# Optimization experiments

Hardware: AMD Instinct MI355X
Metric: run time of the kernel (lower is better)

Reference implementation:

```python
import jax, jax.numpy as jnp
import numpy as np

# ---- static config (must match init_kwargs) ----
DIM = 256
DIM_K = 16
N = 32          # window size: hh = ww = N
HEADS = 8
DIM_OUT = 256
DIM_U = 1
DIM_V = DIM_OUT // HEADS  # 32
EPS = 1e-5
N2 = N * N


def _calc_rel_pos(n):
    # pos: (n*n, 2) of (i, j) coords, rel: (n*n, n*n, 2) shifted by n-1
    pos = np.stack(np.meshgrid(np.arange(n), np.arange(n), indexing='ij'), axis=-1).reshape(-1, 2)
    rel = pos[None, :, :] - pos[:, None, :] + (n - 1)
    return rel.astype(np.int32)

_REL = _calc_rel_pos(N)  # (N2, N2, 2)


def _cplx(re, im):
    return jax.lax.complex(re, im)


def _complex_bn(x, scale, shift):
    # x: (b, c, m) complex. Complex batchnorm: var = E[x^2] - E[x]^2 (complex square).
    mean = x.mean(axis=(0, 2))                       # (c,)
    var = (x ** 2).mean(axis=(0, 2)) - mean ** 2     # (c,) complex
    xn = (x - mean[None, :, None]) / jnp.sqrt(var + EPS)[None, :, None]
    return scale[None, :, None] * xn + shift[None, :, None]


def setup_inputs() -> dict:
    key = jax.random.key(0)
    ks = jax.random.split(key, 18)
    f = jnp.float32
    b = 16
    mk = lambda k, shape, s=1.0: (jax.random.normal(k, shape, dtype=f) * s)
    inp = {
        'x_re': mk(ks[0], (b, DIM, N, N)),
        'x_im': mk(ks[1], (b, DIM, N, N)),
        # 1x1 conv weights, stored as (out_ch, in_ch)
        'wq_re': mk(ks[2], (DIM_K * HEADS, DIM), DIM ** -0.5),
        'wq_im': mk(ks[3], (DIM_K * HEADS, DIM), DIM ** -0.5),
        'wk_re': mk(ks[4], (DIM_K * DIM_U, DIM), DIM ** -0.5),
        'wk_im': mk(ks[5], (DIM_K * DIM_U, DIM), DIM ** -0.5),
        'wv_re': mk(ks[6], (DIM_V * DIM_U, DIM), DIM ** -0.5),
        'wv_im': mk(ks[7], (DIM_V * DIM_U, DIM), DIM ** -0.5),
        # complex BN affine params (init: scale=1+0j, shift=0)
        'qs_re': jnp.ones((DIM_K * HEADS,), f),
        'qs_im': jnp.zeros((DIM_K * HEADS,), f),
        'qb_re': jnp.zeros((DIM_K * HEADS,), f),
        'qb_im': jnp.zeros((DIM_K * HEADS,), f),
        'vs_re': jnp.ones((DIM_V * DIM_U,), f),
        'vs_im': jnp.zeros((DIM_V * DIM_U,), f),
        'vb_re': jnp.zeros((DIM_V * DIM_U,), f),
        'vb_im': jnp.zeros((DIM_V * DIM_U,), f),
        # rel-pos embedding table (2n-1, 2n-1, k, u)
        'emb_re': mk(ks[8], (2 * N - 1, 2 * N - 1, DIM_K, DIM_U)),
        'emb_im': mk(ks[9], (2 * N - 1, 2 * N - 1, DIM_K, DIM_U)),
    }
    return inp


def reference(x_re, x_im, wq_re, wq_im, wk_re, wk_im, wv_re, wv_im,
              qs_re, qs_im, qb_re, qb_im, vs_re, vs_im, vb_re, vb_im,
              emb_re, emb_im):
    x = _cplx(x_re, x_im)                       # (b, c, N, N)
    b = x.shape[0]
    xf = x.reshape(b, DIM, N2)                  # (b, c, m)

    wq = _cplx(wq_re, wq_im)
    wk = _cplx(wk_re, wk_im)
    wv = _cplx(wv_re, wv_im)

    q = jnp.einsum('oc,bcm->bom', wq, xf)       # (b, k*h, m)
    k = jnp.einsum('oc,bcm->bom', wk, xf)       # (b, k*u, m)
    v = jnp.einsum('oc,bcm->bom', wv, xf)       # (b, v*u, m)

    q = _complex_bn(q, _cplx(qs_re, qs_im), _cplx(qb_re, qb_im))
    v = _complex_bn(v, _cplx(vs_re, vs_im), _cplx(vb_re, vb_im))

    q = q.reshape(b, HEADS, DIM_K, N2)          # b h k n
    k = k.reshape(b, DIM_U, DIM_K, N2)          # b u k m
    v = v.reshape(b, DIM_U, DIM_V, N2)          # b u v m

    k = jax.nn.softmax(jnp.abs(k), axis=-1).astype(jnp.complex64)

    lam_c = jnp.einsum('bukm,buvm->bkv', k, v)          # content lambda
    Yc = jnp.einsum('bhkn,bkv->bhvn', q, lam_c)

    emb = _cplx(emb_re, emb_im)
    remb = emb[_REL[..., 0], _REL[..., 1]]              # (n, m, k, u) gathered
    lam_p = jnp.einsum('nmku,buvm->bnkv', remb, v)      # positional lambdas
    Yp = jnp.einsum('bhkn,bnkv->bhvn', q, lam_p)

    Y = Yc + Yp                                          # (b, h, v, n)
    out = Y.reshape(b, HEADS * DIM_V, N, N)             # b (h v) hh ww
    return out
```

## Files before the change

kernel.cpp:

```cpp
#include <hip/hip_runtime.h>
#include <math.h>

#define DIMC 256
#define NCH  176
#define MM   1024
#define BB   16
#define KD   16
#define HH   8
#define VD   32
#define EPSV 1e-5
#define OPAD 192

typedef short short8 __attribute__((ext_vector_type(8)));
typedef float f32x4  __attribute__((ext_vector_type(4)));
typedef unsigned u32x4v __attribute__((ext_vector_type(4)));

union frag8 { unsigned u[4]; short8 s; u32x4v v; };

__device__ __forceinline__ unsigned bf16rne(float f) {
    unsigned u = __float_as_uint(f);
    unsigned r = u + 0x7FFFu + ((u >> 16) & 1u);
    return r >> 16;
}
__device__ __forceinline__ float bf16tof(unsigned h) {
    return __uint_as_float(h << 16);
}

#define GL2LDS16(g, l) __builtin_amdgcn_global_load_lds( \
    (const __attribute__((address_space(1))) unsigned*)(g), \
    (__attribute__((address_space(3))) unsigned*)(l), 16, 0, 0)

__global__ __launch_bounds__(256) void k_wprep(
    const float* __restrict__ wq_re, const float* __restrict__ wq_im,
    const float* __restrict__ wk_re, const float* __restrict__ wk_im,
    const float* __restrict__ wv_re, const float* __restrict__ wv_im,
    unsigned* __restrict__ Wpk)
{
    int idx = blockIdx.x * 256 + threadIdx.x;
    if (idx >= OPAD * 128) return;
    int o = idx >> 7, j = idx & 127;
    int c0 = 2 * j;
    float r0 = 0.f, r1 = 0.f, i0 = 0.f, i1 = 0.f;
    if (o < 128) {
        r0 = wq_re[o * DIMC + c0]; r1 = wq_re[o * DIMC + c0 + 1];
        i0 = wq_im[o * DIMC + c0]; i1 = wq_im[o * DIMC + c0 + 1];
    } else if (o < 144) {
        int oo = o - 128;
        r0 = wk_re[oo * DIMC + c0]; r1 = wk_re[oo * DIMC + c0 + 1];
        i0 = wk_im[oo * DIMC + c0]; i1 = wk_im[oo * DIMC + c0 + 1];
    } else if (o < 176) {
        int oo = o - 144;
        r0 = wv_re[oo * DIMC + c0]; r1 = wv_re[oo * DIMC + c0 + 1];
        i0 = wv_im[oo * DIMC + c0]; i1 = wv_im[oo * DIMC + c0 + 1];
    }
    unsigned rh0 = bf16rne(r0), rh1 = bf16rne(r1);
    unsigned ih0 = bf16rne(i0), ih1 = bf16rne(i1);
    float rl0 = r0 - bf16tof(rh0), rl1 = r1 - bf16tof(rh1);
    float il0 = i0 - bf16tof(ih0), il1 = i1 - bf16tof(ih1);
    Wpk[0 * OPAD * 128 + idx] = rh0 | (rh1 << 16);
    Wpk[1 * OPAD * 128 + idx] = ih0 | (ih1 << 16);
    Wpk[2 * OPAD * 128 + idx] = bf16rne(rl0) | (bf16rne(rl1) << 16);
    Wpk[3 * OPAD * 128 + idx] = bf16rne(il0) | (bf16rne(il1) << 16);
}

__global__ __launch_bounds__(256, 2) void k_proj(
    const float* __restrict__ x_re, const float* __restrict__ x_im,
    const unsigned* __restrict__ Wpk,
    float2* __restrict__ O)
{
    const int m0  = blockIdx.x * 32;
    const int b   = blockIdx.y;
    const int tid = threadIdx.x;
    const int w    = tid >> 6;
    const int lane = tid & 63;
    const int quad = lane >> 4;
    const int col  = lane & 15;
    const int mt = w & 1, og = w >> 1;

    __shared__ __align__(16) unsigned Wsh[4 * OPAD * 16];
    __shared__ __align__(16) unsigned Xsh[4 * 32 * 20];

    f32x4 accR[6], accI[6];
#pragma unroll
    for (int t = 0; t < 6; ++t) {
        accR[t] = (f32x4){0.f, 0.f, 0.f, 0.f};
        accI[t] = (f32x4){0.f, 0.f, 0.f, 0.f};
    }

    const int cl = tid >> 3;
    const int m4 = (tid & 7) * 4;
    const int cp = cl >> 1, half = cl & 1;

#pragma unroll 1
    for (int kk = 0; kk < 8; ++kk) {
#pragma unroll
        for (int p = 0; p < 12; ++p) {
            int idx = p * 256 + tid;
            int plane = idx / 768;
            int rem = idx - plane * 768;
            int row = rem >> 2, seg = rem & 3;
            u32x4v d = *(const u32x4v*)&Wpk[(size_t)plane * (OPAD * 128) + row * 128 + kk * 16 + seg * 4];
            *(u32x4v*)&Wsh[(plane * OPAD + row) * 16 + seg * 4] = d;
        }
        {
            size_t base = ((size_t)(b * DIMC + kk * 32 + cl)) * MM + m0 + m4;
            float4 xr = *(const float4*)&x_re[base];
            float4 xi = *(const float4*)&x_im[base];
            unsigned short* xs = (unsigned short*)Xsh;
            const float* xrf = (const float*)&xr;
            const float* xif = (const float*)&xi;
#pragma unroll
            for (int j = 0; j < 4; ++j) {
                float r = xrf[j], iv = xif[j];
                unsigned rh = bf16rne(r), ih = bf16rne(iv);
                float rl = r - bf16tof(rh), il = iv - bf16tof(ih);
                int m = m4 + j;
                xs[(0 * 640 + m * 20 + cp) * 2 + half] = (unsigned short)rh;
                xs[(1 * 640 + m * 20 + cp) * 2 + half] = (unsigned short)ih;
                xs[(2 * 640 + m * 20 + cp) * 2 + half] = (unsigned short)bf16rne(rl);
                xs[(3 * 640 + m * 20 + cp) * 2 + half] = (unsigned short)bf16rne(il);
            }
        }
        __syncthreads();

        int mrow = mt * 16 + col;
        short8 Xrh = *(const short8*)&Xsh[0 * 640 + mrow * 20 + quad * 4];
        short8 Xih = *(const short8*)&Xsh[1 * 640 + mrow * 20 + quad * 4];
        short8 Xrl = *(const short8*)&Xsh[2 * 640 + mrow * 20 + quad * 4];
        short8 Xil = *(const short8*)&Xsh[3 * 640 + mrow * 20 + quad * 4];

#pragma unroll
        for (int ot = 0; ot < 6; ++ot) {
            int orow = (og * 6 + ot) * 16 + col;
            frag8 Arh, Aih, Arl, Ail, Anh, Anl;
            Arh.s = *(const short8*)&Wsh[(0 * OPAD + orow) * 16 + quad * 4];
            Aih.s = *(const short8*)&Wsh[(1 * OPAD + orow) * 16 + quad * 4];
            Arl.s = *(const short8*)&Wsh[(2 * OPAD + orow) * 16 + quad * 4];
            Ail.s = *(const short8*)&Wsh[(3 * OPAD + orow) * 16 + quad * 4];
#pragma unroll
            for (int i = 0; i < 4; ++i) {
                Anh.u[i] = Aih.u[i] ^ 0x80008000u;
                Anl.u[i] = Ail.u[i] ^ 0x80008000u;
            }
            accR[ot] = __builtin_amdgcn_mfma_f32_16x16x32_bf16(Arh.s, Xrh, accR[ot], 0, 0, 0);
            accR[ot] = __builtin_amdgcn_mfma_f32_16x16x32_bf16(Anh.s, Xih, accR[ot], 0, 0, 0);
            accR[ot] = __builtin_amdgcn_mfma_f32_16x16x32_bf16(Arh.s, Xrl, accR[ot], 0, 0, 0);
            accR[ot] = __builtin_amdgcn_mfma_f32_16x16x32_bf16(Anh.s, Xil, accR[ot], 0, 0, 0);
            accR[ot] = __builtin_amdgcn_mfma_f32_16x16x32_bf16(Arl.s, Xrh, accR[ot], 0, 0, 0);
            accR[ot] = __builtin_amdgcn_mfma_f32_16x16x32_bf16(Anl.s, Xih, accR[ot], 0, 0, 0);
            accI[ot] = __builtin_amdgcn_mfma_f32_16x16x32_bf16(Arh.s, Xih, accI[ot], 0, 0, 0);
            accI[ot] = __builtin_amdgcn_mfma_f32_16x16x32_bf16(Aih.s, Xrh, accI[ot], 0, 0, 0);
            accI[ot] = __builtin_amdgcn_mfma_f32_16x16x32_bf16(Arh.s, Xil, accI[ot], 0, 0, 0);
            accI[ot] = __builtin_amdgcn_mfma_f32_16x16x32_bf16(Aih.s, Xrl, accI[ot], 0, 0, 0);
            accI[ot] = __builtin_amdgcn_mfma_f32_16x16x32_bf16(Arl.s, Xih, accI[ot], 0, 0, 0);
            accI[ot] = __builtin_amdgcn_mfma_f32_16x16x32_bf16(Ail.s, Xrh, accI[ot], 0, 0, 0);
        }
        __syncthreads();
    }

#pragma unroll
    for (int ot = 0; ot < 6; ++ot) {
        int gto = og * 6 + ot;
        if (gto >= 11) continue;
#pragma unroll
        for (int r = 0; r < 4; ++r) {
            int o = gto * 16 + quad * 4 + r;
            O[((size_t)(b * NCH + o)) * MM + m0 + mt * 16 + col] =
                make_float2(accR[ot][r], accI[ot][r]);
        }
    }
}

__global__ __launch_bounds__(256) void k_bnstats(
    const float2* __restrict__ O,
    const float* __restrict__ qs_re, const float* __restrict__ qs_im,
    const float* __restrict__ qb_re, const float* __restrict__ qb_im,
    const float* __restrict__ vs_re, const float* __restrict__ vs_im,
    const float* __restrict__ vb_re, const float* __restrict__ vb_im,
    float4* __restrict__ stats)
{
    const int ch  = blockIdx.x;
    const int o   = (ch < 128) ? ch : (144 + ch - 128);
    const int tid = threadIdx.x;

    double sr = 0, si = 0, sq = 0, sri = 0;
    for (int idx = tid; idx < BB * MM; idx += 256) {
        int b = idx >> 10, m = idx & 1023;
        float2 val = O[((size_t)(b * NCH + o)) * MM + m];
        double r = val.x, ii = val.y;
        sr += r; si += ii; sq += r * r - ii * ii; sri += r * ii;
    }
    __shared__ double red[4][256];
    red[0][tid] = sr; red[1][tid] = si; red[2][tid] = sq; red[3][tid] = sri;
    __syncthreads();
    for (int s = 128; s > 0; s >>= 1) {
        if (tid < s) {
            red[0][tid] += red[0][tid + s]; red[1][tid] += red[1][tid + s];
            red[2][tid] += red[2][tid + s]; red[3][tid] += red[3][tid + s];
        }
        __syncthreads();
    }
    if (tid == 0) {
        const double inv = 1.0 / (double)(BB * MM);
        double mr = red[0][0] * inv, mi = red[1][0] * inv;
        double vr = red[2][0] * inv - (mr * mr - mi * mi) + EPSV;
        double vi = 2.0 * (red[3][0] * inv - mr * mi);
        double rad = sqrt(vr * vr + vi * vi);
        double wr  = sqrt(fmax(0.5 * (rad + vr), 0.0));
        double wi  = sqrt(fmax(0.5 * (rad - vr), 0.0));
        if (vi < 0) wi = -wi;
        double den = wr * wr + wi * wi;
        double ivr = wr / den, ivi = -wi / den;
        double scr, sci, shr, shi;
        if (ch < 128) { scr = qs_re[ch]; sci = qs_im[ch]; shr = qb_re[ch]; shi = qb_im[ch]; }
        else { int i2 = ch - 128; scr = vs_re[i2]; sci = vs_im[i2]; shr = vb_re[i2]; shi = vb_im[i2]; }
        double Ar = scr * ivr - sci * ivi;
        double Ai = scr * ivi + sci * ivr;
        double Br = shr - (Ar * mr - Ai * mi);
        double Bi = shi - (Ar * mi + Ai * mr);
        stats[ch] = make_float4((float)Ar, (float)Ai, (float)Br, (float)Bi);
    }
}

__global__ __launch_bounds__(256) void k_bnapply(
    const float4* __restrict__ stats, float2* __restrict__ O,
    unsigned* __restrict__ VR, unsigned* __restrict__ VI)
{
    int ch = blockIdx.x, b = blockIdx.y;
    int o  = (ch < 128) ? ch : (144 + ch - 128);
    float4 s = stats[ch];
    float2* row = O + ((size_t)(b * NCH + o)) * MM;
    int tid = threadIdx.x;
    for (int mm = tid; mm < 512; mm += 256) {
        float4 two = *(float4*)&row[2 * mm];
        float nr0 = s.x * two.x - s.y * two.y + s.z;
        float ni0 = s.x * two.y + s.y * two.x + s.w;
        float nr1 = s.x * two.z - s.y * two.w + s.z;
        float ni1 = s.x * two.w + s.y * two.z + s.w;
        *(float4*)&row[2 * mm] = make_float4(nr0, ni0, nr1, ni1);
        if (ch >= 128) {
            int bv = b * VD + (ch - 128);
            int cC = mm >> 4, off = mm & 15;
            size_t idx = ((size_t)cC * 512 + bv) * 16 + off;
            VR[idx] = bf16rne(nr0) | (bf16rne(nr1) << 16);
            VI[idx] = bf16rne(ni0) | (bf16rne(ni1) << 16);
        }
    }
}

__global__ __launch_bounds__(256) void k_softlam(
    const float2* __restrict__ O, float2* __restrict__ lamc)
{
    int kc = blockIdx.x, b = blockIdx.y;
    const float2* row = O + ((size_t)(b * NCH + 128 + kc)) * MM;
    int tid = threadIdx.x;
    __shared__ float red[256];
    __shared__ float skl[1024];

    float mag[4]; float mx = -1e30f;
#pragma unroll
    for (int j = 0; j < 4; ++j) {
        float2 v = row[tid + j * 256];
        mag[j] = sqrtf(v.x * v.x + v.y * v.y);
        mx = fmaxf(mx, mag[j]);
    }
    red[tid] = mx; __syncthreads();
    for (int s = 128; s > 0; s >>= 1) { if (tid < s) red[tid] = fmaxf(red[tid], red[tid + s]); __syncthreads(); }
    mx = red[0]; __syncthreads();
    float e[4]; float sum = 0.f;
#pragma unroll
    for (int j = 0; j < 4; ++j) { e[j] = expf(mag[j] - mx); sum += e[j]; }
    red[tid] = sum; __syncthreads();
    for (int s = 128; s > 0; s >>= 1) { if (tid < s) red[tid] += red[tid + s]; __syncthreads(); }
    float inv = 1.f / red[0];
#pragma unroll
    for (int j = 0; j < 4; ++j) skl[tid + j * 256] = e[j] * inv;
    __syncthreads();

    int v = tid >> 3, s8 = tid & 7;
    const float2* vrow = O + ((size_t)(b * NCH + 144 + v)) * MM;
    float ar = 0.f, ai = 0.f;
    for (int i = 0; i < 128; ++i) {
        int m = s8 * 128 + i;
        float wgt = skl[m]; float2 vv = vrow[m];
        ar += wgt * vv.x; ai += wgt * vv.y;
    }
    __shared__ float2 part[32][8];
    part[v][s8] = make_float2(ar, ai);
    __syncthreads();
    if (tid < 32) {
        float2 t = part[tid][0];
#pragma unroll
        for (int j = 1; j < 8; ++j) { t.x += part[tid][j].x; t.y += part[tid][j].y; }
        lamc[((size_t)(b * KD + kc)) * VD + tid] = t;
    }
}

__global__ __launch_bounds__(256) void k_eprepD(
    const float* __restrict__ er, const float* __restrict__ ei,
    unsigned* __restrict__ embD)
{
    int idx = blockIdx.x * 256 + threadIdx.x;
    if (idx >= 8 * 63 * 768) return;
    int s   = idx % 48;
    int k   = (idx / 48) % 16;
    int di  = (idx / 768) % 63;
    int win = idx / (768 * 63);
    int u_s = s >> 2, o = s & 3;
    int p   = (((k >> 1) & 1) << 1) | ((k >> 2) & 1);
    int dj2 = ((u_s ^ p) << 2) | o;
    int dj  = 28 - win * 4 + dj2;
    unsigned val = 0;
    if (dj <= 62) {
        int e = (di * 63 + dj) * 16 + k;
        val = bf16rne(er[e]) | (bf16rne(ei[e]) << 16);
    }
    embD[idx] = val;
}

__global__ __launch_bounds__(256, 2) void k_main(
    const float2* __restrict__ O,
    const unsigned* __restrict__ embD,
    const unsigned* __restrict__ VbfR,
    const unsigned* __restrict__ VbfI,
    const float2* __restrict__ lamc,
    float* __restrict__ out, int cplx)
{
    const int tid  = threadIdx.x;
    const int w    = tid >> 6;
    const int lane = tid & 63;
    const int quad = lane >> 4;
    const int col  = lane & 15;

    const int n0  = blockIdx.x * 4;
    const int bvq = blockIdx.y;
    const int b0  = bvq * 4;
    const int ni  = n0 >> 5;
    const int nj0 = n0 & 31;
    const int win = nj0 >> 2;

    __shared__ __align__(16) unsigned embS[2][768];
    __shared__ __align__(16) float2 lamqs[4096];

    f32x4 accr[4][2], acci[4][2];
#pragma unroll
    for (int g = 0; g < 4; ++g)
#pragma unroll
        for (int t = 0; t < 2; ++t) {
            accr[g][t] = (f32x4){0.f, 0.f, 0.f, 0.f};
            acci[g][t] = (f32x4){0.f, 0.f, 0.f, 0.f};
        }

    const unsigned* vR = VbfR + ((size_t)(bvq * 128 + w * 32 + col)) * 16 + quad * 4;
    const unsigned* vI = VbfI + ((size_t)(bvq * 128 + w * 32 + col)) * 16 + quad * 4;

    const unsigned* eDw = embD + (size_t)win * (63 * 768);

    const int p  = (((col >> 1) & 1) << 1) | ((col >> 2) & 1);
    const int aBase = col * 48;
    const int a0 = aBase + (((2 * quad)     ^ p) << 2);
    const int a1 = aBase + (((2 * quad + 1) ^ p) << 2);
    const int a2 = aBase + (((2 * quad + 2) ^ p) << 2);

    if (w < 3)
        GL2LDS16(eDw + (size_t)(31 - ni) * 768 + w * 256 + lane * 4,
                 (unsigned*)embS[0] + w * 256);
    frag8 cBr0, cBr1, cBi0, cBi1;
    cBr0.v = *(const u32x4v*)(vR);
    cBr1.v = *(const u32x4v*)(vR + 256);
    cBi0.v = *(const u32x4v*)(vI);
    cBi1.v = *(const u32x4v*)(vI + 256);

#pragma unroll 1
    for (int c = 0; c < 32; ++c) {
        __syncthreads();

        const int cn = (c + 1 < 32) ? (c + 1) : 31;
        if (w < 3)
            GL2LDS16(eDw + (size_t)(cn - ni + 31) * 768 + w * 256 + lane * 4,
                     (unsigned*)embS[cn & 1] + w * 256);
        frag8 nBr0, nBr1, nBi0, nBi1;
        {
            const unsigned* r  = vR + (size_t)cn * 8192;
            const unsigned* ii = vI + (size_t)cn * 8192;
            nBr0.v = *(const u32x4v*)(r);
            nBr1.v = *(const u32x4v*)(r + 256);
            nBi0.v = *(const u32x4v*)(ii);
            nBi1.v = *(const u32x4v*)(ii + 256);
        }

        const unsigned* es = (const unsigned*)embS[c & 1];
        u32x4v W0 = *(const u32x4v*)&es[a0];
        u32x4v W1 = *(const u32x4v*)&es[a1];
        u32x4v W2 = *(const u32x4v*)&es[a2];
        unsigned W[12] = { W0.x, W0.y, W0.z, W0.w,
                           W1.x, W1.y, W1.z, W1.w,
                           W2.x, W2.y, W2.z, W2.w };

#pragma unroll
        for (int g = 0; g < 4; ++g) {
            const int o = 3 - g;
            union { unsigned u[4]; short8 s; } Rr, Ri, Rin;
            Rr.u[0] = __builtin_amdgcn_perm(W[o + 1], W[o + 0], 0x05040100u);
            Rr.u[1] = __builtin_amdgcn_perm(W[o + 3], W[o + 2], 0x05040100u);
            Rr.u[2] = __builtin_amdgcn_perm(W[o + 5], W[o + 4], 0x05040100u);
            Rr.u[3] = __builtin_amdgcn_perm(W[o + 7], W[o + 6], 0x05040100u);
            Ri.u[0] = __builtin_amdgcn_perm(W[o + 1], W[o + 0], 0x07060302u);
            Ri.u[1] = __builtin_amdgcn_perm(W[o + 3], W[o + 2], 0x07060302u);
            Ri.u[2] = __builtin_amdgcn_perm(W[o + 5], W[o + 4], 0x07060302u);
            Ri.u[3] = __builtin_amdgcn_perm(W[o + 7], W[o + 6], 0x07060302u);
            Rin.u[0] = Ri.u[0] ^ 0x80008000u;
            Rin.u[1] = Ri.u[1] ^ 0x80008000u;
            Rin.u[2] = Ri.u[2] ^ 0x80008000u;
            Rin.u[3] = Ri.u[3] ^ 0x80008000u;
            accr[g][0] = __builtin_amdgcn_mfma_f32_16x16x32_bf16(Rr.s,  cBr0.s, accr[g][0], 0, 0, 0);
            accr[g][0] = __builtin_amdgcn_mfma_f32_16x16x32_bf16(Rin.s, cBi0.s, accr[g][0], 0, 0, 0);
            acci[g][0] = __builtin_amdgcn_mfma_f32_16x16x32_bf16(Rr.s,  cBi0.s, acci[g][0], 0, 0, 0);
            acci[g][0] = __builtin_amdgcn_mfma_f32_16x16x32_bf16(Ri.s,  cBr0.s, acci[g][0], 0, 0, 0);
            accr[g][1] = __builtin_amdgcn_mfma_f32_16x16x32_bf16(Rr.s,  cBr1.s, accr[g][1], 0, 0, 0);
            accr[g][1] = __builtin_amdgcn_mfma_f32_16x16x32_bf16(Rin.s, cBi1.s, accr[g][1], 0, 0, 0);
            acci[g][1] = __builtin_amdgcn_mfma_f32_16x16x32_bf16(Rr.s,  cBi1.s, acci[g][1], 0, 0, 0);
            acci[g][1] = __builtin_amdgcn_mfma_f32_16x16x32_bf16(Ri.s,  cBr1.s, acci[g][1], 0, 0, 0);
        }
        cBr0 = nBr0; cBr1 = nBr1; cBi0 = nBi0; cBi1 = nBi1;
    }

#pragma unroll
    for (int it = 0; it < 8; ++it) {
        int idx = it * 256 + tid;
        int g = idx & 3, ch = (idx >> 2) & 127, bl = idx >> 9;
        lamqs[2048 + idx] = O[((size_t)((b0 + bl) * NCH + ch)) * MM + n0 + g];
    }

    float2 lcv[2][4];
#pragma unroll
    for (int t = 0; t < 2; ++t) {
        int bvl = w * 32 + t * 16 + col;
        int bloc = b0 + (bvl >> 5), v = bvl & 31;
#pragma unroll
        for (int r = 0; r < 4; ++r)
            lcv[t][r] = lamc[((size_t)(bloc * KD + quad * 4 + r)) * VD + v];
    }

    float2* lamt = lamqs;
    float2* qsh  = lamqs + 2048;
    const int col128 = tid & 127;
    const int hb = (tid >> 7) * 4;
    const int bl = col128 >> 5, vY = col128 & 31;
    const int bY = b0 + bl;
    float2* op2 = (float2*)out;
#pragma unroll
    for (int g = 0; g < 4; ++g) {
        __syncthreads();
#pragma unroll
        for (int t = 0; t < 2; ++t) {
            int bvl = w * 32 + t * 16 + col;
#pragma unroll
            for (int r = 0; r < 4; ++r) {
                int k = quad * 4 + r;
                lamt[k * 128 + bvl] = make_float2(accr[g][t][r] + lcv[t][r].x,
                                                  acci[g][t][r] + lcv[t][r].y);
            }
        }
        __syncthreads();
        float yr[4], yi[4];
#pragma unroll
        for (int h = 0; h < 4; ++h) { yr[h] = 0.f; yi[h] = 0.f; }
#pragma unroll
        for (int k = 0; k < 16; ++k) {
            float2 l = lamt[k * 128 + col128];
#pragma unroll
            for (int h = 0; h < 4; ++h) {
                float2 q = qsh[(bl * 128 + (hb + h) * 16 + k) * 4 + g];
                yr[h] += q.x * l.x - q.y * l.y;
                yi[h] += q.x * l.y + q.y * l.x;
            }
        }
        int n = n0 + g;
        if (cplx) {
#pragma unroll
            for (int h = 0; h < 4; ++h)
                op2[((size_t)(bY * 256 + (hb + h) * 32 + vY)) * MM + n] = make_float2(yr[h], yi[h]);
        } else {
#pragma unroll
            for (int h = 0; h < 4; ++h)
                out[((size_t)(bY * 256 + (hb + h) * 32 + vY)) * MM + n] = yr[h];
        }
    }
}

extern "C" void kernel_launch(void* const* d_in, const int* in_sizes, int n_in,
                              void* d_out, int out_size, void* d_ws, size_t ws_size,
                              hipStream_t stream)
{
    const float* x_re  = (const float*)d_in[0];
    const float* x_im  = (const float*)d_in[1];
    const float* wq_re = (const float*)d_in[2];
    const float* wq_im = (const float*)d_in[3];
    const float* wk_re = (const float*)d_in[4];
    const float* wk_im = (const float*)d_in[5];
    const float* wv_re = (const float*)d_in[6];
    const float* wv_im = (const float*)d_in[7];
    const float* qs_re = (const float*)d_in[8];
    const float* qs_im = (const float*)d_in[9];
    const float* qb_re = (const float*)d_in[10];
    const float* qb_im = (const float*)d_in[11];
    const float* vs_re = (const float*)d_in[12];
    const float* vs_im = (const float*)d_in[13];
    const float* vb_re = (const float*)d_in[14];
    const float* vb_im = (const float*)d_in[15];
    const float* emb_re = (const float*)d_in[16];
    const float* emb_im = (const float*)d_in[17];

    float* ws = (float*)d_ws;
    const size_t O_OFF  = 0;
    const size_t ST_OFF = O_OFF + (size_t)BB * NCH * MM * 2;
    const size_t LC_OFF = ST_OFF + 640;
    const size_t WP_OFF = LC_OFF + 16384;
    const size_t VR_OFF = WP_OFF + 98304;
    const size_t VI_OFF = VR_OFF + 262144;
    const size_t ED_OFF = VI_OFF + 262144;

    float2*   O     = (float2*)(ws + O_OFF);
    float4*   stats = (float4*)(ws + ST_OFF);
    float2*   lamc  = (float2*)(ws + LC_OFF);
    unsigned* Wpk   = (unsigned*)(ws + WP_OFF);
    unsigned* VbfR  = (unsigned*)(ws + VR_OFF);
    unsigned* VbfI  = (unsigned*)(ws + VI_OFF);
    unsigned* embD  = (unsigned*)(ws + ED_OFF);
    float*    outp  = (float*)d_out;

    int cplx = (out_size >= 2 * BB * 256 * MM) ? 1 : 0;

    k_wprep<<<dim3(96), 256, 0, stream>>>(wq_re, wq_im, wk_re, wk_im,
                                          wv_re, wv_im, Wpk);
    k_eprepD<<<dim3(1512), 256, 0, stream>>>(emb_re, emb_im, embD);
    k_proj<<<dim3(32, BB), 256, 0, stream>>>(x_re, x_im, Wpk, O);
    k_bnstats<<<dim3(160), 256, 0, stream>>>(O, qs_re, qs_im, qb_re, qb_im,
                                             vs_re, vs_im, vb_re, vb_im, stats);
    k_bnapply<<<dim3(160, BB), 256, 0, stream>>>(stats, O, VbfR, VbfI);
    k_softlam<<<dim3(KD, BB), 256, 0, stream>>>(O, lamc);
    k_main<<<dim3(256, 4), 256, 0, stream>>>(O, embD, VbfR, VbfI, lamc, outp, cplx);
}
```

Measured before the change: 284.6 us.

## Swizzle weight LDS layout, split BN stats reduction, shrink main kernel shared memory

Three separate changes. The weight tile in k_proj's shared memory now uses an XOR swizzle so the MFMA operand reads hit fewer bank conflicts. The batch-norm statistics pass is split into a partial reduction over a 160x4 grid plus a small finalize kernel, which spreads the reduction over more blocks. In k_main, the embedding double buffer and the lamqs buffer now alias one shared array, and launch bounds are raised to four blocks per SM for higher occupancy. This adds one kernel launch and risks register spilling under the tighter launch bound.

```diff
diff --git a/kernel.cpp b/kernel.cpp
--- a/kernel.cpp
+++ b/kernel.cpp
@@ -99,8 +99,9 @@
             int plane = idx / 768;
             int rem = idx - plane * 768;
             int row = rem >> 2, seg = rem & 3;
+            int sw = (row + (row >> 2)) & 3;
             u32x4v d = *(const u32x4v*)&Wpk[(size_t)plane * (OPAD * 128) + row * 128 + kk * 16 + seg * 4];
-            *(u32x4v*)&Wsh[(plane * OPAD + row) * 16 + seg * 4] = d;
+            *(u32x4v*)&Wsh[(plane * OPAD + row) * 16 + ((seg ^ sw) << 2)] = d;
         }
         {
             size_t base = ((size_t)(b * DIMC + kk * 32 + cl)) * MM + m0 + m4;
@@ -132,11 +133,12 @@
 #pragma unroll
         for (int ot = 0; ot < 6; ++ot) {
             int orow = (og * 6 + ot) * 16 + col;
+            int swq = (quad ^ ((orow + (orow >> 2)) & 3)) << 2;
             frag8 Arh, Aih, Arl, Ail, Anh, Anl;
-            Arh.s = *(const short8*)&Wsh[(0 * OPAD + orow) * 16 + quad * 4];
-            Aih.s = *(const short8*)&Wsh[(1 * OPAD + orow) * 16 + quad * 4];
-            Arl.s = *(const short8*)&Wsh[(2 * OPAD + orow) * 16 + quad * 4];
-            Ail.s = *(const short8*)&Wsh[(3 * OPAD + orow) * 16 + quad * 4];
+            Arh.s = *(const short8*)&Wsh[(0 * OPAD + orow) * 16 + swq];
+            Aih.s = *(const short8*)&Wsh[(1 * OPAD + orow) * 16 + swq];
+            Arl.s = *(const short8*)&Wsh[(2 * OPAD + orow) * 16 + swq];
+            Ail.s = *(const short8*)&Wsh[(3 * OPAD + orow) * 16 + swq];
 #pragma unroll
             for (int i = 0; i < 4; ++i) {
                 Anh.u[i] = Aih.u[i] ^ 0x80008000u;
@@ -171,21 +173,16 @@
     }
 }
 
-__global__ __launch_bounds__(256) void k_bnstats(
-    const float2* __restrict__ O,
-    const float* __restrict__ qs_re, const float* __restrict__ qs_im,
-    const float* __restrict__ qb_re, const float* __restrict__ qb_im,
-    const float* __restrict__ vs_re, const float* __restrict__ vs_im,
-    const float* __restrict__ vb_re, const float* __restrict__ vb_im,
-    float4* __restrict__ stats)
-{
-    const int ch  = blockIdx.x;
-    const int o   = (ch < 128) ? ch : (144 + ch - 128);
+__global__ __launch_bounds__(256) void k_bnstats_part(
+    const float2* __restrict__ O, double* __restrict__ part)
+{
+    const int ch = blockIdx.x, q = blockIdx.y;
+    const int o  = (ch < 128) ? ch : (144 + ch - 128);
     const int tid = threadIdx.x;
 
     double sr = 0, si = 0, sq = 0, sri = 0;
-    for (int idx = tid; idx < BB * MM; idx += 256) {
-        int b = idx >> 10, m = idx & 1023;
+    for (int idx = tid; idx < 4 * MM; idx += 256) {
+        int b = q * 4 + (idx >> 10), m = idx & 1023;
         float2 val = O[((size_t)(b * NCH + o)) * MM + m];
         double r = val.x, ii = val.y;
         sr += r; si += ii; sq += r * r - ii * ii; sri += r * ii;
@@ -201,25 +198,45 @@
         __syncthreads();
     }
     if (tid == 0) {
-        const double inv = 1.0 / (double)(BB * MM);
-        double mr = red[0][0] * inv, mi = red[1][0] * inv;
-        double vr = red[2][0] * inv - (mr * mr - mi * mi) + EPSV;
-        double vi = 2.0 * (red[3][0] * inv - mr * mi);
-        double rad = sqrt(vr * vr + vi * vi);
-        double wr  = sqrt(fmax(0.5 * (rad + vr), 0.0));
-        double wi  = sqrt(fmax(0.5 * (rad - vr), 0.0));
-        if (vi < 0) wi = -wi;
-        double den = wr * wr + wi * wi;
-        double ivr = wr / den, ivi = -wi / den;
-        double scr, sci, shr, shi;
-        if (ch < 128) { scr = qs_re[ch]; sci = qs_im[ch]; shr = qb_re[ch]; shi = qb_im[ch]; }
-        else { int i2 = ch - 128; scr = vs_re[i2]; sci = vs_im[i2]; shr = vb_re[i2]; shi = vb_im[i2]; }
-        double Ar = scr * ivr - sci * ivi;
-        double Ai = scr * ivi + sci * ivr;
-        double Br = shr - (Ar * mr - Ai * mi);
-        double Bi = shi - (Ar * mi + Ai * mr);
-        stats[ch] = make_float4((float)Ar, (float)Ai, (float)Br, (float)Bi);
-    }
+        double* p = part + ((size_t)(ch * 4 + q)) * 4;
+        p[0] = red[0][0]; p[1] = red[1][0]; p[2] = red[2][0]; p[3] = red[3][0];
+    }
+}
+
+__global__ __launch_bounds__(64) void k_bnstats_fin(
+    const double* __restrict__ part,
+    const float* __restrict__ qs_re, const float* __restrict__ qs_im,
+    const float* __restrict__ qb_re, const float* __restrict__ qb_im,
+    const float* __restrict__ vs_re, const float* __restrict__ vs_im,
+    const float* __restrict__ vb_re, const float* __restrict__ vb_im,
+    float4* __restrict__ stats)
+{
+    int ch = blockIdx.x * 64 + threadIdx.x;
+    if (ch >= 160) return;
+    double sr = 0, si = 0, sq = 0, sri = 0;
+#pragma unroll
+    for (int q = 0; q < 4; ++q) {
+        const double* p = part + ((size_t)(ch * 4 + q)) * 4;
+        sr += p[0]; si += p[1]; sq += p[2]; sri += p[3];
+    }
+    const double inv = 1.0 / (double)(BB * MM);
+    double mr = sr * inv, mi = si * inv;
+    double vr = sq * inv - (mr * mr - mi * mi) + EPSV;
+    double vi = 2.0 * (sri * inv - mr * mi);
+    double rad = sqrt(vr * vr + vi * vi);
+    double wr  = sqrt(fmax(0.5 * (rad + vr), 0.0));
+    double wi  = sqrt(fmax(0.5 * (rad - vr), 0.0));
+    if (vi < 0) wi = -wi;
+    double den = wr * wr + wi * wi;
+    double ivr = wr / den, ivi = -wi / den;
+    double scr, sci, shr, shi;
+    if (ch < 128) { scr = qs_re[ch]; sci = qs_im[ch]; shr = qb_re[ch]; shi = qb_im[ch]; }
+    else { int i2 = ch - 128; scr = vs_re[i2]; sci = vs_im[i2]; shr = vb_re[i2]; shi = vb_im[i2]; }
+    double Ar = scr * ivr - sci * ivi;
+    double Ai = scr * ivi + sci * ivr;
+    double Br = shr - (Ar * mr - Ai * mi);
+    double Bi = shi - (Ar * mi + Ai * mr);
+    stats[ch] = make_float4((float)Ar, (float)Ai, (float)Br, (float)Bi);
 }
 
 __global__ __launch_bounds__(256) void k_bnapply(
@@ -318,7 +335,7 @@
     embD[idx] = val;
 }
 
-__global__ __launch_bounds__(256, 2) void k_main(
+__global__ __launch_bounds__(256, 4) void k_main(
     const float2* __restrict__ O,
     const unsigned* __restrict__ embD,
     const unsigned* __restrict__ VbfR,
@@ -339,8 +356,10 @@
     const int nj0 = n0 & 31;
     const int win = nj0 >> 2;
 
-    __shared__ __align__(16) unsigned embS[2][768];
-    __shared__ __align__(16) float2 lamqs[4096];
+    __shared__ __align__(16) unsigned shmem[8192];
+    unsigned* embS0 = shmem;
+    unsigned* embS1 = shmem + 768;
+    float2*   lamqs = (float2*)shmem;
 
     f32x4 accr[4][2], acci[4][2];
 #pragma unroll
@@ -364,7 +383,7 @@
 
     if (w < 3)
         GL2LDS16(eDw + (size_t)(31 - ni) * 768 + w * 256 + lane * 4,
-                 (unsigned*)embS[0] + w * 256);
+                 embS0 + w * 256);
     frag8 cBr0, cBr1, cBi0, cBi1;
     cBr0.v = *(const u32x4v*)(vR);
     cBr1.v = *(const u32x4v*)(vR + 256);
@@ -378,7 +397,7 @@
         const int cn = (c + 1 < 32) ? (c + 1) : 31;
         if (w < 3)
             GL2LDS16(eDw + (size_t)(cn - ni + 31) * 768 + w * 256 + lane * 4,
-                     (unsigned*)embS[cn & 1] + w * 256);
+                     ((cn & 1) ? embS1 : embS0) + w * 256);
         frag8 nBr0, nBr1, nBi0, nBi1;
         {
             const unsigned* r  = vR + (size_t)cn * 8192;
@@ -389,7 +408,7 @@
             nBi1.v = *(const u32x4v*)(ii + 256);
         }
 
-        const unsigned* es = (const unsigned*)embS[c & 1];
+        const unsigned* es = (c & 1) ? embS1 : embS0;
         u32x4v W0 = *(const u32x4v*)&es[a0];
         u32x4v W1 = *(const u32x4v*)&es[a1];
         u32x4v W2 = *(const u32x4v*)&es[a2];
@@ -520,6 +539,7 @@
     const size_t VR_OFF = WP_OFF + 98304;
     const size_t VI_OFF = VR_OFF + 262144;
     const size_t ED_OFF = VI_OFF + 262144;
+    const size_t PT_OFF = ED_OFF + 387072;
 
     float2*   O     = (float2*)(ws + O_OFF);
     float4*   stats = (float4*)(ws + ST_OFF);
@@ -528,6 +548,7 @@
     unsigned* VbfR  = (unsigned*)(ws + VR_OFF);
     unsigned* VbfI  = (unsigned*)(ws + VI_OFF);
     unsigned* embD  = (unsigned*)(ws + ED_OFF);
+    double*   part  = (double*)(ws + PT_OFF);
     float*    outp  = (float*)d_out;
 
     int cplx = (out_size >= 2 * BB * 256 * MM) ? 1 : 0;
@@ -536,8 +557,9 @@
                                           wv_re, wv_im, Wpk);
     k_eprepD<<<dim3(1512), 256, 0, stream>>>(emb_re, emb_im, embD);
     k_proj<<<dim3(32, BB), 256, 0, stream>>>(x_re, x_im, Wpk, O);
-    k_bnstats<<<dim3(160), 256, 0, stream>>>(O, qs_re, qs_im, qb_re, qb_im,
-                                             vs_re, vs_im, vb_re, vb_im, stats);
+    k_bnstats_part<<<dim3(160, 4), 256, 0, stream>>>(O, part);
+    k_bnstats_fin<<<dim3(3), 64, 0, stream>>>(part, qs_re, qs_im, qb_re, qb_im,
+                                              vs_re, vs_im, vb_re, vb_im, stats);
     k_bnapply<<<dim3(160, BB), 256, 0, stream>>>(stats, O, VbfR, VbfI);
     k_softlam<<<dim3(KD, BB), 256, 0, stream>>>(O, lamc);
     k_main<<<dim3(256, 4), 256, 0, stream>>>(O, embD, VbfR, VbfI, lamc, outp, cplx);
```

Result: slower. 340.2 us (+19.5%).
